# Kernel tuning notes

Hardware: AMD Instinct MI355X
Metric: run time of the kernel (lower is better)

Reference implementation:

```python
import jax, jax.numpy as jnp
import numpy as np
import math

B, N, D, H, F, L, T, V = 2, 1024, 256, 8, 1024, 2, 2, 32000
DH = D // H
ALPHA = 0.1  # phase_alpha


def _ln(x, g, b):
    m = jnp.mean(x, -1, keepdims=True)
    v = jnp.mean((x - m) ** 2, -1, keepdims=True)
    return (x - m) * jax.lax.rsqrt(v + 1e-5) * g + b


def setup_inputs() -> dict:
    key = jax.random.key(0)
    ks = iter(jax.random.split(key, 40))
    def nrm(shape, s):
        return jax.random.normal(next(ks), shape, jnp.float32) * s
    s = 1.0 / math.sqrt(D)
    inp = {}
    inp['input_ids'] = jax.random.randint(next(ks), (B, N), 0, V)
    inp['tok_emb'] = nrm((V, D), 0.02)
    inp['pos_emb'] = nrm((N, D), 0.02)
    inp['en_g'] = jnp.ones((D,)); inp['en_b'] = jnp.zeros((D,))
    inp['pi_w'] = nrm((D, H), s); inp['pi_b'] = jnp.zeros((H,))
    inp['Wq'] = nrm((L, D, D), s); inp['Wk'] = nrm((L, D, D), s)
    inp['Wv'] = nrm((L, D, D), s); inp['Wo'] = nrm((L, D, D), s)
    inp['pp_w'] = nrm((L, D, H), s); inp['pp_b'] = jnp.zeros((L, H))
    inp['f1_w'] = nrm((L, D, F), s); inp['f1_b'] = jnp.zeros((L, F))
    inp['f2_w'] = nrm((L, F, D), 1.0 / math.sqrt(F)); inp['f2_b'] = jnp.zeros((L, D))
    inp['ln1_g'] = jnp.ones((L, D)); inp['ln1_b'] = jnp.zeros((L, D))
    inp['ln2_g'] = jnp.ones((L, D)); inp['ln2_b'] = jnp.zeros((L, D))
    inp['pu_w'] = nrm((L, D, H), s); inp['pu_b'] = jnp.zeros((L, H))
    inp['on_g'] = jnp.ones((D,)); inp['on_b'] = jnp.zeros((D,))
    inp['head_w'] = nrm((D, V), s); inp['head_b'] = jnp.zeros((V,))
    return inp


def reference(input_ids, tok_emb, pos_emb, en_g, en_b, pi_w, pi_b,
              Wq, Wk, Wv, Wo, pp_w, pp_b, f1_w, f1_b, f2_w, f2_b,
              ln1_g, ln1_b, ln2_g, ln2_b, pu_w, pu_b, on_g, on_b,
              head_w, head_b):
    # Embedding + positional + LayerNorm (dropout=0 / eval mode)
    h = tok_emb[input_ids] + pos_emb[None, :, :]          # (B,N,D)
    h = _ln(h, en_g, en_b)
    phases = h @ pi_w + pi_b                              # (B,N,H) threaded state
    scale = 1.0 / math.sqrt(DH)
    # Iterated shared-structure blocks (early stop never fires with random init)
    for t in range(T):
        for l in range(L):
            # --- HarmonicEdgeLayer ---
            q = (h @ Wq[l]).reshape(B, N, H, DH)
            k = (h @ Wk[l]).reshape(B, N, H, DH)
            scores = jnp.einsum('bihk,bjhk->bhij', q, k) * scale   # (B,H,N,N)
            ph = (h @ pp_w[l] + pp_b[l]).transpose(0, 2, 1)         # (B,H,N)
            mod = jnp.cos(ph[:, :, :, None] - ph[:, :, None, :])    # (B,H,N,N)
            scores = scores * (1.0 + mod) * 0.5
            ew = jax.nn.softmax(scores, axis=-1)
            # --- HarmonicNodeUpdate ---
            v = (h @ Wv[l]).reshape(B, N, H, DH)
            msg = jnp.einsum('bhij,bjhk->bihk', ew, v).reshape(B, N, D) @ Wo[l]
            h = _ln(h + msg, ln1_g[l], ln1_b[l])
            ff = jax.nn.gelu(h @ f1_w[l] + f1_b[l], approximate=False) @ f2_w[l] + f2_b[l]
            h = _ln(h + ff, ln2_g[l], ln2_b[l])
            # --- PhaseUpdate (state carried; does not feed edge weights) ---
            phases = phases + ALPHA * jnp.tanh(h @ pu_w[l] + pu_b[l]) * math.pi
    h = _ln(h, on_g, on_b)
    pooled = h.mean(axis=1)                               # mean readout, no mask
    return pooled @ head_w + head_b                       # (B, V)
```

## Files before the change

### kernel.cpp

```cpp
#include <hip/hip_runtime.h>
#include <hip/hip_bf16.h>
#include <math.h>

#define DV 256
#define NSEQ 1024
#define HHEADS 8
#define VV 32000
#define QKSCALE 0.17677669529663687f

typedef __attribute__((ext_vector_type(8))) short short8v;
typedef __attribute__((ext_vector_type(4))) float f32x4;

__device__ __forceinline__ unsigned short f2bf(float f){
  __hip_bfloat16 b = __float2bfloat16(f);
  return *reinterpret_cast<unsigned short*>(&b);
}
__device__ __forceinline__ float bfbits2f(unsigned short u){
  unsigned int x = ((unsigned int)u) << 16;
  return __uint_as_float(x);
}

#define OFF_WQKVP 0
#define OFF_WOT   425984
#define OFF_F1T   557056
#define OFF_F2T   1081344
__global__ __launch_bounds__(256) void transpose_cvt_all(
    const float* __restrict__ Wq, const float* __restrict__ Wk,
    const float* __restrict__ Wv, const float* __restrict__ Wo,
    const float* __restrict__ ppw, const float* __restrict__ f1w,
    const float* __restrict__ f2w, __hip_bfloat16* __restrict__ dst){
  __shared__ float sh[32][33];
  int bid = blockIdx.x;
  int t = threadIdx.x;
  if(bid >= 512 && bid < 528){
    int idx = bid - 512;
    int l = idx >> 3, k0 = (idx & 7) * 32;
    int rowo = t >> 2;
    int kbase = k0 + (t & 3) * 8;
    unsigned short vals[8];
    if(rowo < 8){
      int hh = rowo;
      #pragma unroll
      for(int i=0;i<8;i++) vals[i] = f2bf(ppw[(long)l*2048 + (kbase+i)*HHEADS + hh]);
    } else {
      #pragma unroll
      for(int i=0;i<8;i++) vals[i] = 0;
    }
    unsigned short* d = (unsigned short*)dst + (long)l*212992 + (768+rowo)*256 + kbase;
    #pragma unroll
    for(int i=0;i<8;i++) d[i] = vals[i];
    return;
  }
  const float* src; __hip_bfloat16* d; int K, N, tile;
  if(bid < 384){
    int l = bid / 192, rem = bid % 192, mat = rem >> 6; tile = rem & 63;
    src = (mat==0 ? Wq : (mat==1 ? Wk : Wv)) + l*65536;
    d = dst + (long)l*212992 + mat*65536;
    K = 256; N = 256;
  } else if(bid < 512){
    int b2 = bid - 384; int l = b2 >> 6; tile = b2 & 63;
    src = Wo + l*65536; d = dst + OFF_WOT + l*65536; K = 256; N = 256;
  } else if(bid < 1040){
    int b2 = bid - 528; int l = b2 >> 8; tile = b2 & 255;
    src = f1w + l*262144; d = dst + OFF_F1T + l*262144; K = 256; N = 1024;
  } else {
    int b2 = bid - 1040; int l = b2 >> 8; tile = b2 & 255;
    src = f2w + l*262144; d = dst + OFF_F2T + l*262144; K = 1024; N = 256;
  }
  int ntn = N >> 5;
  int tk = tile / ntn, tn = tile - tk*ntn;
  int k0 = tk*32, n0 = tn*32;
  {
    int rr = t >> 3, cc = (t & 7) * 4;
    float4 v = *(const float4*)&src[(long)(k0+rr)*N + n0 + cc];
    sh[rr][cc]=v.x; sh[rr][cc+1]=v.y; sh[rr][cc+2]=v.z; sh[rr][cc+3]=v.w;
  }
  __syncthreads();
  int nn = t >> 3, kk = (t & 7) * 4;
  ushort4 o;
  o.x = f2bf(sh[kk+0][nn]);
  o.y = f2bf(sh[kk+1][nn]);
  o.z = f2bf(sh[kk+2][nn]);
  o.w = f2bf(sh[kk+3][nn]);
  *(ushort4*)&((unsigned short*)d)[(long)(n0+nn)*K + k0 + kk] = o;
}

__global__ __launch_bounds__(256) void embed_kernel(
    const int* __restrict__ ids, const float* __restrict__ tok, const float* __restrict__ pos,
    float* __restrict__ e){
  int t = threadIdx.x;
  int lane = t & 63;
  int row = blockIdx.x*4 + (t >> 6);
  int n = row & (NSEQ-1);
  int id = ids[row];
  float4 vv = ((const float4*)tok)[(long)id*64 + lane];
  float4 pv = ((const float4*)pos)[n*64 + lane];
  vv.x += pv.x; vv.y += pv.y; vv.z += pv.z; vv.w += pv.w;
  ((float4*)e)[row*64 + lane] = vv;
}

template<int ACT, int PHASE>
__global__ __launch_bounds__(256) void gemm_ln(
    const float* __restrict__ Ax, const float* __restrict__ Ar,
    const float* __restrict__ lng, const float* __restrict__ lnb,
    float* __restrict__ hout,
    const __hip_bfloat16* __restrict__ Bt,
    const float* __restrict__ bias,
    __hip_bfloat16* __restrict__ Cout, int N, int ldc,
    const float* __restrict__ pb, float* __restrict__ cph, float* __restrict__ sph){
  __shared__ short As[64][264];
  __shared__ short Bs[64][264];
  int tm = blockIdx.x*64, tn = blockIdx.y*64;
  int t = threadIdx.x;
  int lane = t & 63, w = t >> 6;
  int wm = w >> 1, wn = w & 1;
  int lr = lane & 15, lg = lane >> 4;
  const short* gB = (const short*)Bt;
  {
    int rb = t >> 2, cb = t & 3;
    const short* pbp = &gB[(long)(tn+rb)*DV];
    #pragma unroll
    for(int j=0;j<8;j++){
      int c8 = cb + 4*j;
      *(short8v*)&Bs[rb][c8*8] = *(const short8v*)&pbp[c8*8];
    }
  }
  {
    int r8 = t >> 3;
    int c8 = (t & 7) * 4;
    bool wh = (hout != nullptr) && (blockIdx.y == 0);
    #pragma unroll
    for(int g=0; g<2; g++){
      int row = g*32 + r8;
      const float* xr = Ax + (long)(tm+row)*DV;
      const float* rr = Ar ? Ar + (long)(tm+row)*DV : nullptr;
      float v[32];
      float s=0.f, s2=0.f;
      #pragma unroll
      for(int i=0;i<8;i++){
        float4 xv = *(const float4*)&xr[c8 + 32*i];
        if(rr){
          float4 rv = *(const float4*)&rr[c8 + 32*i];
          xv.x+=rv.x; xv.y+=rv.y; xv.z+=rv.z; xv.w+=rv.w;
        }
        v[4*i]=xv.x; v[4*i+1]=xv.y; v[4*i+2]=xv.z; v[4*i+3]=xv.w;
        s  += xv.x+xv.y+xv.z+xv.w;
        s2 += xv.x*xv.x+xv.y*xv.y+xv.z*xv.z+xv.w*xv.w;
      }
      s += __shfl_xor(s,1); s2 += __shfl_xor(s2,1);
      s += __shfl_xor(s,2); s2 += __shfl_xor(s2,2);
      s += __shfl_xor(s,4); s2 += __shfl_xor(s2,4);
      float mean = s * (1.f/DV);
      float var = fmaxf(s2*(1.f/DV) - mean*mean, 0.f);
      float inv = rsqrtf(var + 1e-5f);
      #pragma unroll
      for(int i=0;i<8;i++){
        int col = c8 + 32*i;
        float4 gv = *(const float4*)&lng[col];
        float4 bv = *(const float4*)&lnb[col];
        float o0 = (v[4*i+0]-mean)*inv*gv.x + bv.x;
        float o1 = (v[4*i+1]-mean)*inv*gv.y + bv.y;
        float o2 = (v[4*i+2]-mean)*inv*gv.z + bv.z;
        float o3 = (v[4*i+3]-mean)*inv*gv.w + bv.w;
        ushort4 ob; ob.x=f2bf(o0); ob.y=f2bf(o1); ob.z=f2bf(o2); ob.w=f2bf(o3);
        *(ushort4*)&As[row][col] = ob;
        if(wh) *(float4*)&hout[(long)(tm+row)*DV + col] = make_float4(o0,o1,o2,o3);
      }
    }
  }
  __syncthreads();
  f32x4 acc[2][2] = {};
  #pragma unroll
  for(int ks=0; ks<8; ks++){
    short8v af[2], bf[2];
    #pragma unroll
    for(int i=0;i<2;i++) af[i] = *(const short8v*)&As[wm*32 + i*16 + lr][ks*32 + lg*8];
    #pragma unroll
    for(int j=0;j<2;j++) bf[j] = *(const short8v*)&Bs[wn*32 + j*16 + lr][ks*32 + lg*8];
    #pragma unroll
    for(int i=0;i<2;i++)
      #pragma unroll
      for(int j=0;j<2;j++)
        acc[i][j] = __builtin_amdgcn_mfma_f32_16x16x32_bf16(af[i], bf[j], acc[i][j], 0,0,0);
  }
  if(PHASE && tn >= N - 64){
    #pragma unroll
    for(int fn=0; fn<2; fn++){
      int colr = wn*32 + fn*16 + lr;
      if(colr < 8){
        float bb = pb[colr];
        #pragma unroll
        for(int fm=0; fm<2; fm++){
          int row0 = tm + wm*32 + fm*16 + lg*4;
          #pragma unroll
          for(int r2=0; r2<4; r2++){
            float ph = acc[fm][fn][r2] + bb;
            float sv, cv;
            __sincosf(ph, &sv, &cv);
            int row = row0 + r2;
            int b = row >> 10, n = row & 1023;
            int idx = (b*HHEADS + colr)*NSEQ + n;
            cph[idx] = cv; sph[idx] = sv;
          }
        }
      }
    }
    return;
  }
  #pragma unroll
  for(int fn=0; fn<2; fn++){
    int col = tn + wn*32 + fn*16 + lr;
    float bs = bias ? bias[col] : 0.f;
    #pragma unroll
    for(int fm=0; fm<2; fm++){
      int row0 = tm + wm*32 + fm*16 + lg*4;
      #pragma unroll
      for(int r2=0; r2<4; r2++){
        float xx = acc[fm][fn][r2] + bs;
        if(ACT == 1) xx = 0.5f*xx*(1.f + erff(xx*0.70710678118654752f));
        Cout[(long)(row0+r2)*ldc + col] = __float2bfloat16(xx);
      }
    }
  }
}

template<int WM, int WN, int FM, int FN, int ACT, int OUT_BF16>
__global__ __launch_bounds__(256) void mfma_gemm(
    const __hip_bfloat16* __restrict__ A, const __hip_bfloat16* __restrict__ Bt,
    const float* __restrict__ bias, void* __restrict__ Cout,
    int M, int N, int K, int ldc){
  constexpr int BM = WM*FM*16;
  constexpr int BN = WN*FN*16;
  constexpr int TPRA = 256/BM;
  constexpr int JA = 16/TPRA;
  __shared__ short As[2][BM][136];
  __shared__ short Bs[2][BN][136];
  int tm = blockIdx.x*BM, tn = blockIdx.y*BN;
  int t = threadIdx.x;
  int lane = t & 63, w = t >> 6;
  int wm = w / WN, wn = w % WN;
  int lr = lane & 15, lg = lane >> 4;
  f32x4 acc[FM][FN] = {};
  const short* gA = (const short*)A;
  const short* gB = (const short*)Bt;
  int ra = t / TPRA, ca = t % TPRA;
  int rb = t >> 2,  cb = t & 3;
  short8v ar[JA], br[4];
#define LOADC(K0) { const short* pa = &gA[(long)(tm+ra)*K + (K0)]; \
    _Pragma("unroll") for(int j=0;j<JA;j++) ar[j] = *(const short8v*)&pa[(ca+TPRA*j)*8]; \
    const short* pbp = &gB[(long)(tn+rb)*K + (K0)]; \
    _Pragma("unroll") for(int j=0;j<4;j++) br[j] = *(const short8v*)&pbp[(cb+4*j)*8]; }
#define STOREC(BUF) { _Pragma("unroll") for(int j=0;j<JA;j++) *(short8v*)&As[BUF][ra][(ca+TPRA*j)*8] = ar[j]; \
    _Pragma("unroll") for(int j=0;j<4;j++) *(short8v*)&Bs[BUF][rb][(cb+4*j)*8] = br[j]; }
  int nch = K >> 7;
  LOADC(0);
  STOREC(0);
  if(nch > 1) LOADC(128);
  __syncthreads();
  for(int c=0; c<nch; c++){
    int cur = c & 1;
    #pragma unroll
    for(int ks=0; ks<4; ks++){
      short8v af[FM], bf[FN];
      #pragma unroll
      for(int i=0;i<FM;i++) af[i] = *(const short8v*)&As[cur][wm*FM*16 + i*16 + lr][ks*32 + lg*8];
      #pragma unroll
      for(int j=0;j<FN;j++) bf[j] = *(const short8v*)&Bs[cur][wn*FN*16 + j*16 + lr][ks*32 + lg*8];
      #pragma unroll
      for(int i=0;i<FM;i++)
        #pragma unroll
        for(int j=0;j<FN;j++)
          acc[i][j] = __builtin_amdgcn_mfma_f32_16x16x32_bf16(af[i], bf[j], acc[i][j], 0,0,0);
    }
    if(c+1 < nch){
      STOREC(cur^1);
      if(c+2 < nch) LOADC((c+2)*128);
    }
    __syncthreads();
  }
#undef LOADC
#undef STOREC
  #pragma unroll
  for(int fn=0; fn<FN; fn++){
    int col = tn + wn*FN*16 + fn*16 + lr;
    float bs = bias ? bias[col] : 0.f;
    #pragma unroll
    for(int fm=0; fm<FM; fm++){
      int row0 = tm + wm*FM*16 + fm*16 + lg*4;
      #pragma unroll
      for(int r2=0; r2<4; r2++){
        float xx = acc[fm][fn][r2] + bs;
        if(ACT == 1) xx = 0.5f*xx*(1.f + erff(xx*0.70710678118654752f));
        long idx = (long)(row0+r2)*ldc + col;
        if(OUT_BF16) ((__hip_bfloat16*)Cout)[idx] = __float2bfloat16(xx);
        else         ((float*)Cout)[idx] = xx;
      }
    }
  }
}

__global__ __launch_bounds__(256) void attn_mfma_kernel(
    const __hip_bfloat16* __restrict__ qkv,
    const float* __restrict__ cph, const float* __restrict__ sph,
    __hip_bfloat16* __restrict__ po, float* __restrict__ ml){
  __shared__ __align__(16) short K2[2][64][104];
  __shared__ __align__(16) short V2[2][32][72];
  __shared__ __align__(16) short Pp[4][16][72];
  int bid = blockIdx.x;
  int bh = bid >> 5;
  int qt = (bid >> 1) & 15;
  int ks = bid & 1;
  int b = bh >> 3, hh = bh & 7;
  int t = threadIdx.x;
  int lane = t & 63, w = t >> 6;
  int lr = lane & 15, lg = lane >> 4;
  int q0w = qt*64 + w*16;

  const unsigned short* qrow = (const unsigned short*)qkv
      + ((long)(b*NSEQ + q0w + lr))*768 + hh*32 + lg*8;
  short8v qraw = *(const short8v*)qrow;
  float ci = cph[bh*NSEQ + q0w + lr];
  float si = sph[bh*NSEQ + q0w + lr];
  short8v qf0, qf1, qf2;
  #pragma unroll
  for(int i=0;i<8;i++){
    float x = bfbits2f((unsigned short)qraw[i]) * (0.5f*QKSCALE);
    qf0[i] = (short)f2bf(x);
    qf1[i] = (short)f2bf(x*ci);
    qf2[i] = (short)f2bf(x*si);
  }

  int srow = t >> 2, sdc = (t & 3) * 8;
  int j0b = ks*8;
  short8v kv, vvr; float cj, sj;
#define LOADT(J) { long rg = (long)(b*NSEQ + (J)*64 + srow)*768; \
    kv  = *(const short8v*)((const unsigned short*)qkv + rg + 256 + hh*32 + sdc); \
    vvr = *(const short8v*)((const unsigned short*)qkv + rg + 512 + hh*32 + sdc); \
    cj = cph[bh*NSEQ + (J)*64 + srow]; sj = sph[bh*NSEQ + (J)*64 + srow]; }
#define STORET(BUF) { short8v kc, ksv; \
    _Pragma("unroll") for(int i=0;i<8;i++){ float x = bfbits2f((unsigned short)kv[i]); \
      kc[i] = (short)f2bf(x*cj); ksv[i] = (short)f2bf(x*sj); } \
    *(short8v*)&K2[BUF][srow][sdc]    = kv; \
    *(short8v*)&K2[BUF][srow][32+sdc] = kc; \
    *(short8v*)&K2[BUF][srow][64+sdc] = ksv; \
    _Pragma("unroll") for(int i=0;i<8;i++) V2[BUF][sdc+i][srow] = vvr[i]; }

  float l = 0.f;
  f32x4 acc[2] = {};

  LOADT(j0b);
  STORET(0);
  LOADT(j0b+1);
  __syncthreads();
  for(int j=0; j<8; j++){
    int cur = j & 1;
    f32x4 st[4];
    #pragma unroll
    for(int kt=0; kt<4; kt++){
      short8v a0 = *(const short8v*)&K2[cur][kt*16+lr][lg*8];
      short8v a1 = *(const short8v*)&K2[cur][kt*16+lr][32+lg*8];
      short8v a2 = *(const short8v*)&K2[cur][kt*16+lr][64+lg*8];
      f32x4 z = {0.f,0.f,0.f,0.f};
      z = __builtin_amdgcn_mfma_f32_16x16x32_bf16(a0, qf0, z, 0,0,0);
      z = __builtin_amdgcn_mfma_f32_16x16x32_bf16(a1, qf1, z, 0,0,0);
      z = __builtin_amdgcn_mfma_f32_16x16x32_bf16(a2, qf2, z, 0,0,0);
      st[kt] = z;
    }
    float ls = 0.f;
    #pragma unroll
    for(int kt=0; kt<4; kt++){
      float p0 = __expf(st[kt][0]);
      float p1 = __expf(st[kt][1]);
      float p2 = __expf(st[kt][2]);
      float p3 = __expf(st[kt][3]);
      ls += (p0+p1)+(p2+p3);
      unsigned int w0 = (unsigned)f2bf(p0) | ((unsigned)f2bf(p1)<<16);
      unsigned int w1 = (unsigned)f2bf(p2) | ((unsigned)f2bf(p3)<<16);
      unsigned int* pp = (unsigned int*)&Pp[w][lr][kt*16 + lg*4];
      pp[0] = w0; pp[1] = w1;
    }
    ls += __shfl_xor(ls, 16);
    ls += __shfl_xor(ls, 32);
    l += ls;
    #pragma unroll
    for(int kk=0; kk<2; kk++){
      short8v pa  = *(const short8v*)&Pp[w][lr][kk*32 + lg*8];
      short8v vf0 = *(const short8v*)&V2[cur][lr][kk*32 + lg*8];
      short8v vf1 = *(const short8v*)&V2[cur][16+lr][kk*32 + lg*8];
      acc[0] = __builtin_amdgcn_mfma_f32_16x16x32_bf16(pa, vf0, acc[0], 0,0,0);
      acc[1] = __builtin_amdgcn_mfma_f32_16x16x32_bf16(pa, vf1, acc[1], 0,0,0);
    }
    if(j < 7){
      STORET(cur^1);
      if(j < 6) LOADT(j0b+j+2);
    }
    __syncthreads();
  }
#undef LOADT
#undef STORET
  if(lane < 16){
    ml[((long)(ks*16+bh))*NSEQ + q0w + lr] = l;
  }
  #pragma unroll
  for(int dt=0; dt<2; dt++)
    #pragma unroll
    for(int r=0;r<4;r++){
      int row = q0w + lg*4 + r;
      po[(((long)(ks*16+bh))*NSEQ + row)*32 + dt*16 + lr] =
          __float2bfloat16(acc[dt][r]);
    }
}

__global__ __launch_bounds__(256) void wo_gemm(
    const __hip_bfloat16* __restrict__ po, const float* __restrict__ ml,
    const __hip_bfloat16* __restrict__ Bt, float* __restrict__ Cout){
  __shared__ short As[32][264];
  __shared__ short Bs[64][264];
  int tm = blockIdx.x*32, tn = blockIdx.y*64;
  int t = threadIdx.x;
  int lane = t & 63, w = t >> 6;
  int lr = lane & 15, lg = lane >> 4;
  const short* gB = (const short*)Bt;
  {
    int rb = t >> 2, cb = t & 3;
    const short* pbp = &gB[(long)(tn+rb)*256];
    #pragma unroll
    for(int j=0;j<8;j++){
      int c8 = cb + 4*j;
      *(short8v*)&Bs[rb][c8*8] = *(const short8v*)&pbp[c8*8];
    }
  }
  {
    int r = t >> 3, hd = t & 7;
    int R = tm + r; int b = R >> 10, q = R & 1023;
    int bh = b*HHEADS + hd;
    float l1 = ml[(long)bh*NSEQ + q];
    float l2 = ml[(long)(16+bh)*NSEQ + q];
    float inv = 1.f/(l1+l2);
    const unsigned short* p1 = (const unsigned short*)po + ((long)bh*NSEQ + q)*32;
    const unsigned short* p2 = (const unsigned short*)po + ((long)(16+bh)*NSEQ + q)*32;
    #pragma unroll
    for(int i=0;i<4;i++){
      short8v a1 = *(const short8v*)&p1[i*8];
      short8v a2 = *(const short8v*)&p2[i*8];
      short8v o;
      #pragma unroll
      for(int k=0;k<8;k++)
        o[k] = (short)f2bf((bfbits2f((unsigned short)a1[k]) + bfbits2f((unsigned short)a2[k]))*inv);
      *(short8v*)&As[r][hd*32 + i*8] = o;
    }
  }
  __syncthreads();
  f32x4 acc[2] = {};
  #pragma unroll
  for(int ksx=0; ksx<8; ksx++){
    short8v af0 = *(const short8v*)&As[lr][ksx*32 + lg*8];
    short8v af1 = *(const short8v*)&As[16+lr][ksx*32 + lg*8];
    short8v bf0 = *(const short8v*)&Bs[w*16+lr][ksx*32 + lg*8];
    acc[0] = __builtin_amdgcn_mfma_f32_16x16x32_bf16(af0, bf0, acc[0], 0,0,0);
    acc[1] = __builtin_amdgcn_mfma_f32_16x16x32_bf16(af1, bf0, acc[1], 0,0,0);
  }
  int col = tn + w*16 + lr;
  #pragma unroll
  for(int fm=0; fm<2; fm++){
    int row0 = tm + fm*16 + lg*4;
    #pragma unroll
    for(int r2=0; r2<4; r2++)
      Cout[(long)(row0+r2)*256 + col] = acc[fm][r2];
  }
}

__global__ __launch_bounds__(256) void final_pool_kernel(
    const float* __restrict__ x, const float* __restrict__ r,
    const float* __restrict__ g2, const float* __restrict__ b2,
    const float* __restrict__ og, const float* __restrict__ ob,
    float* __restrict__ part){
  __shared__ float ws2[32][260];
  int t = threadIdx.x;
  int lrow = t >> 3;
  int row = blockIdx.x*32 + lrow;
  int c0 = (t & 7) * 32;
  float v[32];
  float s=0.f, s2=0.f;
  const float* xr = x + (long)row*DV + c0;
  const float* rr = r + (long)row*DV + c0;
  #pragma unroll
  for(int i=0;i<8;i++){
    float4 xv = *(const float4*)&xr[4*i];
    float4 rv = *(const float4*)&rr[4*i];
    xv.x+=rv.x; xv.y+=rv.y; xv.z+=rv.z; xv.w+=rv.w;
    v[4*i]=xv.x; v[4*i+1]=xv.y; v[4*i+2]=xv.z; v[4*i+3]=xv.w;
    s += xv.x+xv.y+xv.z+xv.w;
    s2 += xv.x*xv.x+xv.y*xv.y+xv.z*xv.z+xv.w*xv.w;
  }
  s += __shfl_xor(s,1); s2 += __shfl_xor(s2,1);
  s += __shfl_xor(s,2); s2 += __shfl_xor(s2,2);
  s += __shfl_xor(s,4); s2 += __shfl_xor(s2,4);
  float mean = s*(1.f/DV);
  float var = fmaxf(s2*(1.f/DV)-mean*mean, 0.f);
  float inv = rsqrtf(var + 1e-5f);
  float s_=0.f, s2_=0.f;
  #pragma unroll
  for(int i=0;i<32;i++){
    int col = c0 + i;
    float o = (v[i]-mean)*inv*g2[col] + b2[col];
    v[i] = o;
    s_ += o; s2_ += o*o;
  }
  s_ += __shfl_xor(s_,1); s2_ += __shfl_xor(s2_,1);
  s_ += __shfl_xor(s_,2); s2_ += __shfl_xor(s2_,2);
  s_ += __shfl_xor(s_,4); s2_ += __shfl_xor(s2_,4);
  float mean2 = s_*(1.f/DV);
  float var2 = fmaxf(s2_*(1.f/DV)-mean2*mean2, 0.f);
  float inv2 = rsqrtf(var2 + 1e-5f);
  #pragma unroll
  for(int i=0;i<32;i++){
    int col = c0 + i;
    ws2[lrow][col] = (v[i]-mean2)*inv2*og[col] + ob[col];
  }
  __syncthreads();
  float accv = 0.f;
  #pragma unroll 8
  for(int rr2=0; rr2<32; rr2++) accv += ws2[rr2][t];
  part[blockIdx.x*DV + t] = accv;
}

__global__ __launch_bounds__(256) void head_kernel(
    const float* __restrict__ part, const float* __restrict__ W,
    const float* __restrict__ hb, float* __restrict__ out){
  __shared__ float pooled[2][256];
  int t = threadIdx.x;
  float a0 = 0.f, a1 = 0.f;
  #pragma unroll 8
  for(int k=0;k<32;k++){ a0 += part[k*DV + t]; a1 += part[(32+k)*DV + t]; }
  pooled[0][t] = a0 * (1.f/NSEQ);
  pooled[1][t] = a1 * (1.f/NSEQ);
  __syncthreads();
  int vcol = blockIdx.x*256 + t;
  float x0 = 0.f, x1 = 0.f;
  #pragma unroll 8
  for(int d=0; d<DV; d++){
    float wv = W[(long)d*VV + vcol];
    x0 += pooled[0][d]*wv;
    x1 += pooled[1][d]*wv;
  }
  float bb = hb[vcol];
  out[vcol] = x0 + bb;
  out[VV + vcol] = x1 + bb;
}

extern "C" void kernel_launch(void* const* d_in, const int* in_sizes, int n_in,
                              void* d_out, int out_size, void* d_ws, size_t ws_size,
                              hipStream_t stream){
  const int*   ids   = (const int*)  d_in[0];
  const float* tok   = (const float*)d_in[1];
  const float* pos   = (const float*)d_in[2];
  const float* en_g  = (const float*)d_in[3];
  const float* en_b  = (const float*)d_in[4];
  const float* Wq    = (const float*)d_in[7];
  const float* Wk    = (const float*)d_in[8];
  const float* Wv    = (const float*)d_in[9];
  const float* Wo    = (const float*)d_in[10];
  const float* pp_w  = (const float*)d_in[11];
  const float* pp_b  = (const float*)d_in[12];
  const float* f1_w  = (const float*)d_in[13];
  const float* f1_b  = (const float*)d_in[14];
  const float* f2_w  = (const float*)d_in[15];
  const float* f2_b  = (const float*)d_in[16];
  const float* ln1_g = (const float*)d_in[17];
  const float* ln1_b = (const float*)d_in[18];
  const float* ln2_g = (const float*)d_in[19];
  const float* ln2_b = (const float*)d_in[20];
  const float* on_g  = (const float*)d_in[23];
  const float* on_b  = (const float*)d_in[24];
  const float* head_w= (const float*)d_in[25];
  const float* head_b= (const float*)d_in[26];
  float* out = (float*)d_out;

  char* wsb = (char*)d_ws;
  float* s_ff = (float*)(wsb);
  float* hB   = (float*)(wsb + (2u<<20));
  float* s_wo = (float*)(wsb + (4u<<20));
  __hip_bfloat16* qkv = (__hip_bfloat16*)(wsb + (6u<<20));
  __hip_bfloat16* po  = (__hip_bfloat16*)(wsb + (9u<<20));
  float* mlb  = (float*)(wsb + (11u<<20));
  float* hA   = (float*)(wsb + (12u<<20));
  __hip_bfloat16* ff  = (__hip_bfloat16*)(wsb + (14u<<20));
  float* cphb = (float*)(wsb + (18u<<20));
  float* sphb = cphb + 16384;
  float* part = sphb + 16384;
  __hip_bfloat16* wt = (__hip_bfloat16*)(wsb + (18u<<20) + (192u<<10));
  __hip_bfloat16* wqkvp = wt + OFF_WQKVP;
  __hip_bfloat16* wot   = wt + OFF_WOT;
  __hip_bfloat16* f1t   = wt + OFF_F1T;
  __hip_bfloat16* f2t   = wt + OFF_F2T;

  transpose_cvt_all<<<1552, 256, 0, stream>>>(Wq, Wk, Wv, Wo, pp_w, f1_w, f2_w, wt);
  embed_kernel<<<512, 256, 0, stream>>>(ids, tok, pos, s_ff);

  const float* lnPg = en_g;
  const float* lnPb = en_b;
  const float* rres = nullptr;
  for(int it=0; it<4; it++){
    int l = it & 1;
    gemm_ln<0,1><<<dim3(32,13), 256, 0, stream>>>(
        s_ff, rres, lnPg, lnPb, hA,
        wqkvp + (long)l*212992, nullptr, qkv, 832, 768,
        pp_b + l*HHEADS, cphb, sphb);
    attn_mfma_kernel<<<512, 256, 0, stream>>>(qkv, cphb, sphb, po, mlb);
    wo_gemm<<<dim3(64,4), 256, 0, stream>>>(po, mlb, wot + l*65536, s_wo);
    gemm_ln<1,0><<<dim3(32,16), 256, 0, stream>>>(
        s_wo, hA, ln1_g + l*DV, ln1_b + l*DV, hB,
        f1t + l*262144, f1_b + l*1024, ff, 1024, 1024,
        nullptr, nullptr, nullptr);
    mfma_gemm<1,4,2,1, 0,0><<<dim3(64,4), 256, 0, stream>>>(
        ff, f2t + l*262144, f2_b + l*DV, s_ff, 2048, 256, 1024, 256);
    lnPg = ln2_g + l*DV; lnPb = ln2_b + l*DV; rres = hB;
  }
  final_pool_kernel<<<64, 256, 0, stream>>>(s_ff, hB, ln2_g + DV, ln2_b + DV, on_g, on_b, part);
  head_kernel<<<125, 256, 0, stream>>>(part, head_w, head_b, out);
}
```

Measured before the change: 234.7 us.

## Restructure LayerNorm placement, split attention keys four ways, fuse Wo with LN1

```diff
diff --git a/kernel.cpp b/kernel.cpp
--- a/kernel.cpp
+++ b/kernel.cpp
@@ -85,9 +85,10 @@
   *(ushort4*)&((unsigned short*)d)[(long)(n0+nn)*K + k0 + kk] = o;
 }
 
-__global__ __launch_bounds__(256) void embed_kernel(
+__global__ __launch_bounds__(256) void embed_ln_kernel(
     const int* __restrict__ ids, const float* __restrict__ tok, const float* __restrict__ pos,
-    float* __restrict__ e){
+    const float* __restrict__ g, const float* __restrict__ bt,
+    float* __restrict__ h, __hip_bfloat16* __restrict__ hb){
   int t = threadIdx.x;
   int lane = t & 63;
   int row = blockIdx.x*4 + (t >> 6);
@@ -96,139 +97,56 @@
   float4 vv = ((const float4*)tok)[(long)id*64 + lane];
   float4 pv = ((const float4*)pos)[n*64 + lane];
   vv.x += pv.x; vv.y += pv.y; vv.z += pv.z; vv.w += pv.w;
-  ((float4*)e)[row*64 + lane] = vv;
-}
-
-template<int ACT, int PHASE>
-__global__ __launch_bounds__(256) void gemm_ln(
-    const float* __restrict__ Ax, const float* __restrict__ Ar,
-    const float* __restrict__ lng, const float* __restrict__ lnb,
-    float* __restrict__ hout,
-    const __hip_bfloat16* __restrict__ Bt,
-    const float* __restrict__ bias,
-    __hip_bfloat16* __restrict__ Cout, int N, int ldc,
-    const float* __restrict__ pb, float* __restrict__ cph, float* __restrict__ sph){
-  __shared__ short As[64][264];
-  __shared__ short Bs[64][264];
-  int tm = blockIdx.x*64, tn = blockIdx.y*64;
-  int t = threadIdx.x;
-  int lane = t & 63, w = t >> 6;
-  int wm = w >> 1, wn = w & 1;
-  int lr = lane & 15, lg = lane >> 4;
-  const short* gB = (const short*)Bt;
-  {
-    int rb = t >> 2, cb = t & 3;
-    const short* pbp = &gB[(long)(tn+rb)*DV];
-    #pragma unroll
-    for(int j=0;j<8;j++){
-      int c8 = cb + 4*j;
-      *(short8v*)&Bs[rb][c8*8] = *(const short8v*)&pbp[c8*8];
-    }
-  }
-  {
-    int r8 = t >> 3;
-    int c8 = (t & 7) * 4;
-    bool wh = (hout != nullptr) && (blockIdx.y == 0);
-    #pragma unroll
-    for(int g=0; g<2; g++){
-      int row = g*32 + r8;
-      const float* xr = Ax + (long)(tm+row)*DV;
-      const float* rr = Ar ? Ar + (long)(tm+row)*DV : nullptr;
-      float v[32];
-      float s=0.f, s2=0.f;
-      #pragma unroll
-      for(int i=0;i<8;i++){
-        float4 xv = *(const float4*)&xr[c8 + 32*i];
-        if(rr){
-          float4 rv = *(const float4*)&rr[c8 + 32*i];
-          xv.x+=rv.x; xv.y+=rv.y; xv.z+=rv.z; xv.w+=rv.w;
-        }
-        v[4*i]=xv.x; v[4*i+1]=xv.y; v[4*i+2]=xv.z; v[4*i+3]=xv.w;
-        s  += xv.x+xv.y+xv.z+xv.w;
-        s2 += xv.x*xv.x+xv.y*xv.y+xv.z*xv.z+xv.w*xv.w;
-      }
-      s += __shfl_xor(s,1); s2 += __shfl_xor(s2,1);
-      s += __shfl_xor(s,2); s2 += __shfl_xor(s2,2);
-      s += __shfl_xor(s,4); s2 += __shfl_xor(s2,4);
-      float mean = s * (1.f/DV);
-      float var = fmaxf(s2*(1.f/DV) - mean*mean, 0.f);
-      float inv = rsqrtf(var + 1e-5f);
-      #pragma unroll
-      for(int i=0;i<8;i++){
-        int col = c8 + 32*i;
-        float4 gv = *(const float4*)&lng[col];
-        float4 bv = *(const float4*)&lnb[col];
-        float o0 = (v[4*i+0]-mean)*inv*gv.x + bv.x;
-        float o1 = (v[4*i+1]-mean)*inv*gv.y + bv.y;
-        float o2 = (v[4*i+2]-mean)*inv*gv.z + bv.z;
-        float o3 = (v[4*i+3]-mean)*inv*gv.w + bv.w;
-        ushort4 ob; ob.x=f2bf(o0); ob.y=f2bf(o1); ob.z=f2bf(o2); ob.w=f2bf(o3);
-        *(ushort4*)&As[row][col] = ob;
-        if(wh) *(float4*)&hout[(long)(tm+row)*DV + col] = make_float4(o0,o1,o2,o3);
-      }
-    }
-  }
-  __syncthreads();
-  f32x4 acc[2][2] = {};
-  #pragma unroll
-  for(int ks=0; ks<8; ks++){
-    short8v af[2], bf[2];
-    #pragma unroll
-    for(int i=0;i<2;i++) af[i] = *(const short8v*)&As[wm*32 + i*16 + lr][ks*32 + lg*8];
-    #pragma unroll
-    for(int j=0;j<2;j++) bf[j] = *(const short8v*)&Bs[wn*32 + j*16 + lr][ks*32 + lg*8];
-    #pragma unroll
-    for(int i=0;i<2;i++)
-      #pragma unroll
-      for(int j=0;j<2;j++)
-        acc[i][j] = __builtin_amdgcn_mfma_f32_16x16x32_bf16(af[i], bf[j], acc[i][j], 0,0,0);
-  }
-  if(PHASE && tn >= N - 64){
-    #pragma unroll
-    for(int fn=0; fn<2; fn++){
-      int colr = wn*32 + fn*16 + lr;
-      if(colr < 8){
-        float bb = pb[colr];
-        #pragma unroll
-        for(int fm=0; fm<2; fm++){
-          int row0 = tm + wm*32 + fm*16 + lg*4;
-          #pragma unroll
-          for(int r2=0; r2<4; r2++){
-            float ph = acc[fm][fn][r2] + bb;
-            float sv, cv;
-            __sincosf(ph, &sv, &cv);
-            int row = row0 + r2;
-            int b = row >> 10, n = row & 1023;
-            int idx = (b*HHEADS + colr)*NSEQ + n;
-            cph[idx] = cv; sph[idx] = sv;
-          }
-        }
-      }
-    }
-    return;
-  }
-  #pragma unroll
-  for(int fn=0; fn<2; fn++){
-    int col = tn + wn*32 + fn*16 + lr;
-    float bs = bias ? bias[col] : 0.f;
-    #pragma unroll
-    for(int fm=0; fm<2; fm++){
-      int row0 = tm + wm*32 + fm*16 + lg*4;
-      #pragma unroll
-      for(int r2=0; r2<4; r2++){
-        float xx = acc[fm][fn][r2] + bs;
-        if(ACT == 1) xx = 0.5f*xx*(1.f + erff(xx*0.70710678118654752f));
-        Cout[(long)(row0+r2)*ldc + col] = __float2bfloat16(xx);
-      }
-    }
-  }
-}
-
-template<int WM, int WN, int FM, int FN, int ACT, int OUT_BF16>
+  float s  = vv.x+vv.y+vv.z+vv.w;
+  float s2 = vv.x*vv.x+vv.y*vv.y+vv.z*vv.z+vv.w*vv.w;
+  #pragma unroll
+  for(int off=1; off<64; off<<=1){ s += __shfl_xor(s, off); s2 += __shfl_xor(s2, off); }
+  float mean = s*(1.f/DV);
+  float var = fmaxf(s2*(1.f/DV) - mean*mean, 0.f);
+  float inv = rsqrtf(var + 1e-5f);
+  float4 gv = ((const float4*)g)[lane];
+  float4 bv = ((const float4*)bt)[lane];
+  float4 o;
+  o.x=(vv.x-mean)*inv*gv.x+bv.x; o.y=(vv.y-mean)*inv*gv.y+bv.y;
+  o.z=(vv.z-mean)*inv*gv.z+bv.z; o.w=(vv.w-mean)*inv*gv.w+bv.w;
+  ((float4*)h)[row*64 + lane] = o;
+  ushort4 ob; ob.x=f2bf(o.x); ob.y=f2bf(o.y); ob.z=f2bf(o.z); ob.w=f2bf(o.w);
+  *(ushort4*)&hb[row*DV + lane*4] = ob;
+}
+
+__global__ __launch_bounds__(256) void ln_res_kernel(
+    const float* __restrict__ x, const float* __restrict__ r,
+    float* __restrict__ out, __hip_bfloat16* __restrict__ outb,
+    const float* __restrict__ g, const float* __restrict__ bt){
+  int t = threadIdx.x;
+  int lane = t & 63;
+  int row = blockIdx.x*4 + (t >> 6);
+  float4 vv = ((const float4*)x)[row*64 + lane];
+  float4 rv = ((const float4*)r)[row*64 + lane];
+  vv.x += rv.x; vv.y += rv.y; vv.z += rv.z; vv.w += rv.w;
+  float s  = vv.x+vv.y+vv.z+vv.w;
+  float s2 = vv.x*vv.x+vv.y*vv.y+vv.z*vv.z+vv.w*vv.w;
+  #pragma unroll
+  for(int off=1; off<64; off<<=1){ s += __shfl_xor(s, off); s2 += __shfl_xor(s2, off); }
+  float mean = s*(1.f/DV);
+  float var = fmaxf(s2*(1.f/DV) - mean*mean, 0.f);
+  float inv = rsqrtf(var + 1e-5f);
+  float4 gv = ((const float4*)g)[lane];
+  float4 bv = ((const float4*)bt)[lane];
+  float4 o;
+  o.x=(vv.x-mean)*inv*gv.x+bv.x; o.y=(vv.y-mean)*inv*gv.y+bv.y;
+  o.z=(vv.z-mean)*inv*gv.z+bv.z; o.w=(vv.w-mean)*inv*gv.w+bv.w;
+  ((float4*)out)[row*64 + lane] = o;
+  ushort4 ob; ob.x=f2bf(o.x); ob.y=f2bf(o.y); ob.z=f2bf(o.z); ob.w=f2bf(o.w);
+  *(ushort4*)&outb[row*DV + lane*4] = ob;
+}
+
+template<int WM, int WN, int FM, int FN, int ACT, int OUT_BF16, int PHASE>
 __global__ __launch_bounds__(256) void mfma_gemm(
     const __hip_bfloat16* __restrict__ A, const __hip_bfloat16* __restrict__ Bt,
     const float* __restrict__ bias, void* __restrict__ Cout,
-    int M, int N, int K, int ldc){
+    int M, int N, int K, int ldc,
+    const float* __restrict__ pb, float* __restrict__ cph, float* __restrict__ sph){
   constexpr int BM = WM*FM*16;
   constexpr int BN = WN*FN*16;
   constexpr int TPRA = 256/BM;
@@ -280,6 +198,30 @@
   }
 #undef LOADC
 #undef STOREC
+  if(PHASE && tn >= N - 64){
+    #pragma unroll
+    for(int fn=0; fn<FN; fn++){
+      int colr = wn*FN*16 + fn*16 + lr;
+      if(colr < 8){
+        float bb = pb[colr];
+        #pragma unroll
+        for(int fm=0; fm<FM; fm++){
+          int row0 = tm + wm*FM*16 + fm*16 + lg*4;
+          #pragma unroll
+          for(int r2=0; r2<4; r2++){
+            float ph = acc[fm][fn][r2] + bb;
+            float sv, cv;
+            __sincosf(ph, &sv, &cv);
+            int row = row0 + r2;
+            int b = row >> 10, n = row & 1023;
+            int idx = (b*HHEADS + colr)*NSEQ + n;
+            cph[idx] = cv; sph[idx] = sv;
+          }
+        }
+      }
+    }
+    return;
+  }
   #pragma unroll
   for(int fn=0; fn<FN; fn++){
     int col = tn + wn*FN*16 + fn*16 + lr;
@@ -307,9 +249,9 @@
   __shared__ __align__(16) short V2[2][32][72];
   __shared__ __align__(16) short Pp[4][16][72];
   int bid = blockIdx.x;
-  int bh = bid >> 5;
-  int qt = (bid >> 1) & 15;
-  int ks = bid & 1;
+  int bh = bid >> 6;
+  int qt = (bid >> 2) & 15;
+  int ks = bid & 3;
   int b = bh >> 3, hh = bh & 7;
   int t = threadIdx.x;
   int lane = t & 63, w = t >> 6;
@@ -331,7 +273,7 @@
   }
 
   int srow = t >> 2, sdc = (t & 3) * 8;
-  int j0b = ks*8;
+  int j0b = ks*4;
   short8v kv, vvr; float cj, sj;
 #define LOADT(J) { long rg = (long)(b*NSEQ + (J)*64 + srow)*768; \
     kv  = *(const short8v*)((const unsigned short*)qkv + rg + 256 + hh*32 + sdc); \
@@ -352,7 +294,7 @@
   STORET(0);
   LOADT(j0b+1);
   __syncthreads();
-  for(int j=0; j<8; j++){
+  for(int j=0; j<4; j++){
     int cur = j & 1;
     f32x4 st[4];
     #pragma unroll
@@ -390,9 +332,9 @@
       acc[0] = __builtin_amdgcn_mfma_f32_16x16x32_bf16(pa, vf0, acc[0], 0,0,0);
       acc[1] = __builtin_amdgcn_mfma_f32_16x16x32_bf16(pa, vf1, acc[1], 0,0,0);
     }
-    if(j < 7){
+    if(j < 3){
       STORET(cur^1);
-      if(j < 6) LOADT(j0b+j+2);
+      if(j < 2) LOADT(j0b+j+2);
     }
     __syncthreads();
   }
@@ -411,62 +353,110 @@
     }
 }
 
-__global__ __launch_bounds__(256) void wo_gemm(
+__global__ __launch_bounds__(256) void wo_ln_kernel(
     const __hip_bfloat16* __restrict__ po, const float* __restrict__ ml,
-    const __hip_bfloat16* __restrict__ Bt, float* __restrict__ Cout){
-  __shared__ short As[32][264];
+    const __hip_bfloat16* __restrict__ Bt, const float* __restrict__ hres,
+    const float* __restrict__ lng, const float* __restrict__ lnb,
+    float* __restrict__ h1, __hip_bfloat16* __restrict__ hb1){
+  __shared__ short As[16][264];
   __shared__ short Bs[64][264];
-  int tm = blockIdx.x*32, tn = blockIdx.y*64;
+  __shared__ float Co[16][260];
+  int tm = blockIdx.x*16;
   int t = threadIdx.x;
   int lane = t & 63, w = t >> 6;
   int lr = lane & 15, lg = lane >> 4;
+  {
+    int r = t >> 4;
+    int c16 = (t & 15) * 16;
+    int R = tm + r; int b = R >> 10, q = R & 1023;
+    int bh = b*HHEADS + (c16 >> 5);
+    long mlb = (long)bh*NSEQ + q;
+    float lsum = ml[mlb] + ml[mlb + 16*NSEQ] + ml[mlb + 32*NSEQ] + ml[mlb + 48*NSEQ];
+    float inv = 1.f/lsum;
+    long pob = ((long)bh*NSEQ + q)*32 + (c16 & 31);
+    const unsigned short* pp = (const unsigned short*)po;
+    #pragma unroll
+    for(int i=0;i<2;i++){
+      short8v a0 = *(const short8v*)&pp[pob + i*8];
+      short8v a1 = *(const short8v*)&pp[pob + (long)16*NSEQ*32 + i*8];
+      short8v a2 = *(const short8v*)&pp[pob + (long)32*NSEQ*32 + i*8];
+      short8v a3 = *(const short8v*)&pp[pob + (long)48*NSEQ*32 + i*8];
+      short8v o;
+      #pragma unroll
+      for(int k=0;k<8;k++)
+        o[k] = (short)f2bf((bfbits2f((unsigned short)a0[k]) + bfbits2f((unsigned short)a1[k])
+                          + bfbits2f((unsigned short)a2[k]) + bfbits2f((unsigned short)a3[k]))*inv);
+      *(short8v*)&As[r][c16 + i*8] = o;
+    }
+  }
   const short* gB = (const short*)Bt;
+  int rb = t >> 2, cb = t & 3;
   {
-    int rb = t >> 2, cb = t & 3;
-    const short* pbp = &gB[(long)(tn+rb)*256];
-    #pragma unroll
-    for(int j=0;j<8;j++){
-      int c8 = cb + 4*j;
-      *(short8v*)&Bs[rb][c8*8] = *(const short8v*)&pbp[c8*8];
-    }
-  }
+    const short* pbp = &gB[(long)rb*256];
+    #pragma unroll
+    for(int j=0;j<8;j++) *(short8v*)&Bs[rb][(cb+4*j)*8] = *(const short8v*)&pbp[(cb+4*j)*8];
+  }
+  __syncthreads();
+  f32x4 acc[4] = {};
+  for(int ct=0; ct<4; ct++){
+    #pragma unroll
+    for(int ksx=0; ksx<8; ksx++){
+      short8v af = *(const short8v*)&As[lr][ksx*32 + lg*8];
+      short8v bf = *(const short8v*)&Bs[w*16+lr][ksx*32 + lg*8];
+      acc[ct] = __builtin_amdgcn_mfma_f32_16x16x32_bf16(af, bf, acc[ct], 0,0,0);
+    }
+    if(ct < 3){
+      __syncthreads();
+      const short* pbp = &gB[(long)((ct+1)*64 + rb)*256];
+      #pragma unroll
+      for(int j=0;j<8;j++) *(short8v*)&Bs[rb][(cb+4*j)*8] = *(const short8v*)&pbp[(cb+4*j)*8];
+      __syncthreads();
+    }
+  }
+  #pragma unroll
+  for(int ct=0; ct<4; ct++)
+    #pragma unroll
+    for(int r2=0; r2<4; r2++)
+      Co[lg*4 + r2][ct*64 + w*16 + lr] = acc[ct][r2];
+  __syncthreads();
   {
-    int r = t >> 3, hd = t & 7;
-    int R = tm + r; int b = R >> 10, q = R & 1023;
-    int bh = b*HHEADS + hd;
-    float l1 = ml[(long)bh*NSEQ + q];
-    float l2 = ml[(long)(16+bh)*NSEQ + q];
-    float inv = 1.f/(l1+l2);
-    const unsigned short* p1 = (const unsigned short*)po + ((long)bh*NSEQ + q)*32;
-    const unsigned short* p2 = (const unsigned short*)po + ((long)(16+bh)*NSEQ + q)*32;
+    int r = t >> 4;
+    int c16 = (t & 15) * 16;
+    int R = tm + r;
+    float v[16];
+    float s = 0.f, s2 = 0.f;
+    const float* hr = hres + (long)R*DV + c16;
     #pragma unroll
     for(int i=0;i<4;i++){
-      short8v a1 = *(const short8v*)&p1[i*8];
-      short8v a2 = *(const short8v*)&p2[i*8];
-      short8v o;
-      #pragma unroll
-      for(int k=0;k<8;k++)
-        o[k] = (short)f2bf((bfbits2f((unsigned short)a1[k]) + bfbits2f((unsigned short)a2[k]))*inv);
-      *(short8v*)&As[r][hd*32 + i*8] = o;
-    }
-  }
-  __syncthreads();
-  f32x4 acc[2] = {};
-  #pragma unroll
-  for(int ksx=0; ksx<8; ksx++){
-    short8v af0 = *(const short8v*)&As[lr][ksx*32 + lg*8];
-    short8v af1 = *(const short8v*)&As[16+lr][ksx*32 + lg*8];
-    short8v bf0 = *(const short8v*)&Bs[w*16+lr][ksx*32 + lg*8];
-    acc[0] = __builtin_amdgcn_mfma_f32_16x16x32_bf16(af0, bf0, acc[0], 0,0,0);
-    acc[1] = __builtin_amdgcn_mfma_f32_16x16x32_bf16(af1, bf0, acc[1], 0,0,0);
-  }
-  int col = tn + w*16 + lr;
-  #pragma unroll
-  for(int fm=0; fm<2; fm++){
-    int row0 = tm + fm*16 + lg*4;
-    #pragma unroll
-    for(int r2=0; r2<4; r2++)
-      Cout[(long)(row0+r2)*256 + col] = acc[fm][r2];
+      float4 hv = *(const float4*)&hr[4*i];
+      float x0 = Co[r][c16+4*i]   + hv.x;
+      float x1 = Co[r][c16+4*i+1] + hv.y;
+      float x2 = Co[r][c16+4*i+2] + hv.z;
+      float x3 = Co[r][c16+4*i+3] + hv.w;
+      v[4*i]=x0; v[4*i+1]=x1; v[4*i+2]=x2; v[4*i+3]=x3;
+      s += x0+x1+x2+x3;
+      s2 += x0*x0+x1*x1+x2*x2+x3*x3;
+    }
+    s += __shfl_xor(s,1); s2 += __shfl_xor(s2,1);
+    s += __shfl_xor(s,2); s2 += __shfl_xor(s2,2);
+    s += __shfl_xor(s,4); s2 += __shfl_xor(s2,4);
+    s += __shfl_xor(s,8); s2 += __shfl_xor(s2,8);
+    float mean = s*(1.f/DV);
+    float var = fmaxf(s2*(1.f/DV) - mean*mean, 0.f);
+    float invs = rsqrtf(var + 1e-5f);
+    #pragma unroll
+    for(int i=0;i<4;i++){
+      int col = c16 + 4*i;
+      float4 gv = *(const float4*)&lng[col];
+      float4 bv = *(const float4*)&lnb[col];
+      float o0 = (v[4*i+0]-mean)*invs*gv.x + bv.x;
+      float o1 = (v[4*i+1]-mean)*invs*gv.y + bv.y;
+      float o2 = (v[4*i+2]-mean)*invs*gv.z + bv.z;
+      float o3 = (v[4*i+3]-mean)*invs*gv.w + bv.w;
+      *(float4*)&h1[(long)R*DV + col] = make_float4(o0,o1,o2,o3);
+      ushort4 ob; ob.x=f2bf(o0); ob.y=f2bf(o1); ob.z=f2bf(o2); ob.w=f2bf(o3);
+      *(ushort4*)&hb1[(long)R*DV + col] = ob;
+    }
   }
 }
 
@@ -578,45 +568,44 @@
   float* out = (float*)d_out;
 
   char* wsb = (char*)d_ws;
-  float* s_ff = (float*)(wsb);
-  float* hB   = (float*)(wsb + (2u<<20));
-  float* s_wo = (float*)(wsb + (4u<<20));
+  float* h    = (float*)(wsb);
+  __hip_bfloat16* hb  = (__hip_bfloat16*)(wsb + (2u<<20));
+  float* h1   = (float*)(wsb + (3u<<20));
+  __hip_bfloat16* hb1 = (__hip_bfloat16*)(wsb + (5u<<20));
   __hip_bfloat16* qkv = (__hip_bfloat16*)(wsb + (6u<<20));
   __hip_bfloat16* po  = (__hip_bfloat16*)(wsb + (9u<<20));
-  float* mlb  = (float*)(wsb + (11u<<20));
-  float* hA   = (float*)(wsb + (12u<<20));
+  float* mlb  = (float*)(wsb + (13u<<20));
   __hip_bfloat16* ff  = (__hip_bfloat16*)(wsb + (14u<<20));
-  float* cphb = (float*)(wsb + (18u<<20));
+  float* s_ff = (float*)(wsb + (18u<<20));
+  float* cphb = (float*)(wsb + (20u<<20));
   float* sphb = cphb + 16384;
   float* part = sphb + 16384;
-  __hip_bfloat16* wt = (__hip_bfloat16*)(wsb + (18u<<20) + (192u<<10));
+  __hip_bfloat16* wt = (__hip_bfloat16*)(wsb + (20u<<20) + (192u<<10));
   __hip_bfloat16* wqkvp = wt + OFF_WQKVP;
   __hip_bfloat16* wot   = wt + OFF_WOT;
   __hip_bfloat16* f1t   = wt + OFF_F1T;
   __hip_bfloat16* f2t   = wt + OFF_F2T;
 
   transpose_cvt_all<<<1552, 256, 0, stream>>>(Wq, Wk, Wv, Wo, pp_w, f1_w, f2_w, wt);
-  embed_kernel<<<512, 256, 0, stream>>>(ids, tok, pos, s_ff);
-
-  const float* lnPg = en_g;
-  const float* lnPb = en_b;
-  const float* rres = nullptr;
+  embed_ln_kernel<<<512, 256, 0, stream>>>(ids, tok, pos, en_g, en_b, h, hb);
+
   for(int it=0; it<4; it++){
     int l = it & 1;
-    gemm_ln<0,1><<<dim3(32,13), 256, 0, stream>>>(
-        s_ff, rres, lnPg, lnPb, hA,
-        wqkvp + (long)l*212992, nullptr, qkv, 832, 768,
+    mfma_gemm<2,2,2,2, 0,1,1><<<dim3(32,13), 256, 0, stream>>>(
+        hb, wqkvp + (long)l*212992, nullptr, qkv, 2048, 832, 256, 768,
         pp_b + l*HHEADS, cphb, sphb);
-    attn_mfma_kernel<<<512, 256, 0, stream>>>(qkv, cphb, sphb, po, mlb);
-    wo_gemm<<<dim3(64,4), 256, 0, stream>>>(po, mlb, wot + l*65536, s_wo);
-    gemm_ln<1,0><<<dim3(32,16), 256, 0, stream>>>(
-        s_wo, hA, ln1_g + l*DV, ln1_b + l*DV, hB,
-        f1t + l*262144, f1_b + l*1024, ff, 1024, 1024,
+    attn_mfma_kernel<<<1024, 256, 0, stream>>>(qkv, cphb, sphb, po, mlb);
+    wo_ln_kernel<<<128, 256, 0, stream>>>(
+        po, mlb, wot + l*65536, h, ln1_g + l*DV, ln1_b + l*DV, h1, hb1);
+    mfma_gemm<2,2,2,2, 1,1,0><<<dim3(32,16), 256, 0, stream>>>(
+        hb1, f1t + l*262144, f1_b + l*1024, ff, 2048, 1024, 256, 1024,
         nullptr, nullptr, nullptr);
-    mfma_gemm<1,4,2,1, 0,0><<<dim3(64,4), 256, 0, stream>>>(
-        ff, f2t + l*262144, f2_b + l*DV, s_ff, 2048, 256, 1024, 256);
-    lnPg = ln2_g + l*DV; lnPb = ln2_b + l*DV; rres = hB;
-  }
-  final_pool_kernel<<<64, 256, 0, stream>>>(s_ff, hB, ln2_g + DV, ln2_b + DV, on_g, on_b, part);
+    mfma_gemm<1,4,2,1, 0,0,0><<<dim3(64,4), 256, 0, stream>>>(
+        ff, f2t + l*262144, f2_b + l*DV, s_ff, 2048, 256, 1024, 256,
+        nullptr, nullptr, nullptr);
+    if(it < 3)
+      ln_res_kernel<<<512, 256, 0, stream>>>(s_ff, h1, h, hb, ln2_g + l*DV, ln2_b + l*DV);
+  }
+  final_pool_kernel<<<64, 256, 0, stream>>>(s_ff, h1, ln2_g + DV, ln2_b + DV, on_g, on_b, part);
   head_kernel<<<125, 256, 0, stream>>>(part, head_w, head_b, out);
 }
```

Result: faster. 205.8 us (-12.3%).
